# Performance work log

Hardware: AMD Instinct MI355X
Metric: run time of the kernel (lower is better)

## Reference

```python
import jax, jax.numpy as jnp
import numpy as np

B, N = 256, 2000          # clouds, points per cloud
M1, M2 = 100, 5           # fps sample counts (ratio 0.05 twice)
K1, K2 = 20, 20           # neighbors per cluster (= 1/ratio)
R1, R2, R3 = 0.3, 1.0, 2.0
F1, F2, F3 = 5, 25, 45


def _fps(pts, m):
    # iterative farthest point sampling, deterministic start at index 0
    n = pts.shape[0]
    def step(carry, _):
        mind, last = carry
        d = jnp.sum((pts - pts[last]) ** 2, axis=-1)
        mind = jnp.minimum(mind, d)
        return (mind, jnp.argmax(mind).astype(jnp.int32)), last
    _, idx = jax.lax.scan(step, (jnp.full((n,), 1e10, pts.dtype), jnp.int32(0)), None, length=m)
    return idx


def _radius_knn(q, pts, k, r):
    # k nearest neighbors of each query, masked to the radius ball (static-shape gnn.radius)
    d = jnp.sum((q[:, None, :] - pts[None, :, :]) ** 2, axis=-1)  # (M, n)
    negd, idx = jax.lax.top_k(-d, k)
    return idx, (-negd) <= r * r


def _masked_max(h, mask):
    return jnp.max(jnp.where(mask[..., None], h, -1e10), axis=1)


def _forward(points, W1, b1, W2, b2, W3, b3, D1, bD1, D2, bD2, D3, bD3):
    def per_cloud(pts):
        # ---- encode level 1 ----
        samples = pts[_fps(pts, M1)]                              # (M1,3)
        idx1, m1 = _radius_knn(samples, pts, K1, R1)
        rel = (pts[idx1] - samples[:, None, :]) / R1 * m1[..., None]   # (M1,K1,3)
        f1 = _masked_max(jax.nn.relu(rel @ W1 + b1), m1)          # (M1,F1)
        # ---- encode level 2 ----
        samples2 = samples[_fps(samples, M2)]                     # (M2,3)
        idx2, m2 = _radius_knn(samples2, samples, K2, R2)
        rel2 = (samples[idx2] - samples2[:, None, :]) / R2 * m2[..., None]
        h2 = jax.nn.relu(jnp.concatenate([rel2, f1[idx2]], axis=-1) @ W2 + b2)
        f2 = _masked_max(h2, m2)                                  # (M2,F2)
        # ---- encode level 3 (global) ----
        rel3 = samples2 / R3
        h3 = jax.nn.relu(jnp.concatenate([rel3, f2], axis=-1) @ W3 + b3)
        latent = jnp.max(h3, axis=0)                              # (F3,)
        # ---- hierarchical decode ----
        o1 = (latent @ D1 + bD1).reshape(M2, 3 + F2)
        dec, cf = o1[:, :3], jax.nn.relu(o1[:, 3:])               # (M2,3),(M2,F2)
        o2 = (cf @ D2 + bD2).reshape(M2 * K2, 3 + F1)
        dec2, cf2 = o2[:, :3], jax.nn.relu(o2[:, 3:])             # (M2*K2,3/F1)
        dec3 = (cf2 @ D3 + bD3).reshape(M2 * K2 * K1, 3)
        # ---- reconstruction: repeat_interleave + add + scale ----
        s2_out = dec * R3
        s_out = (jnp.repeat(s2_out, K2, axis=0) + dec2) * R2
        return (jnp.repeat(s_out, K1, axis=0) + dec3) * R1        # (N,3)
    return jax.vmap(per_cloud)(points).reshape(B * N, 3)


def setup_inputs():
    key = jax.random.key(0)
    ks = jax.random.split(key, 8)
    p = lambda k, s: jax.random.normal(k, s, jnp.float32) * 0.1
    z = lambda s: jnp.zeros((s,), jnp.float32)
    return {
        "points": jax.random.normal(ks[0], (B, N, 3), jnp.float32),
        "W1": p(ks[1], (3, F1)), "b1": z(F1),
        "W2": p(ks[2], (3 + F1, F2)), "b2": z(F2),
        "W3": p(ks[3], (3 + F2, F3)), "b3": z(F3),
        "D1": p(ks[4], (F3, M2 * (3 + F2))), "bD1": z(M2 * (3 + F2)),
        "D2": p(ks[5], (F2, K2 * (3 + F1))), "bD2": z(K2 * (3 + F1)),
        "D3": p(ks[6], (F1, K1 * 3)), "bD3": z(K1 * 3),
    }


def reference(points, W1, b1, W2, b2, W3, b3, D1, bD1, D2, bD2, D3, bD3):
    return _forward(points, W1, b1, W2, b2, W3, b3, D1, bD1, D2, bD2, D3, bD3)
```

## Files before the change

kernel.cpp:

```cpp
#include <hip/hip_runtime.h>

#define TPB 512
#define NW 8
#define NPTS 2000
#define M1C 100
#define M2C 5
#define KNN 20
#define CAP 64
#define CANDCAP 128

__device__ __forceinline__ float dist3(float px, float py, float pz,
                                       float qx, float qy, float qz) {
#pragma clang fp contract(off)
    float dx = px - qx, dy = py - qy, dz = pz - qz;
    return dx * dx + dy * dy + dz * dz;
}
__device__ __forceinline__ float dist3d(float px, float py, float pz,
                                        float qx, float qy, float qz,
                                        float& dx, float& dy, float& dz) {
#pragma clang fp contract(off)
    dx = px - qx; dy = py - qy; dz = pz - qz;
    return dx * dx + dy * dy + dz * dz;
}

#define ARGMAX_STEP(ctrl, rm)                                                        \
    do {                                                                             \
        float ov = __int_as_float(__builtin_amdgcn_update_dpp(                       \
            (int)0xff800000, __float_as_int(v), ctrl, rm, 0xf, false));              \
        int oi = __builtin_amdgcn_update_dpp(0x7fffffff, i, ctrl, rm, 0xf, false);   \
        bool take = (ov > v) || (ov == v && oi < i);                                 \
        v = take ? ov : v;                                                           \
        i = take ? oi : i;                                                           \
    } while (0)

__device__ __forceinline__ void wave_argmax(float& v, int& i) {
    ARGMAX_STEP(0x111, 0xf);
    ARGMAX_STEP(0x112, 0xf);
    ARGMAX_STEP(0x114, 0xf);
    ARGMAX_STEP(0x118, 0xf);
    ARGMAX_STEP(0x142, 0xa);
    ARGMAX_STEP(0x143, 0xc);
    v = __int_as_float(__builtin_amdgcn_readlane(__float_as_int(v), 63));
    i = __builtin_amdgcn_readlane(i, 63);
}

#define FMAX_STEP(ctrl, rm)                                                          \
    do {                                                                             \
        float _t = __int_as_float(__builtin_amdgcn_update_dpp(                       \
            (int)0xff800000, __float_as_int(x), ctrl, rm, 0xf, false));              \
        x = fmaxf(x, _t);                                                            \
    } while (0)

__device__ __forceinline__ float wave_fmax(float x) {
    FMAX_STEP(0x111, 0xf);
    FMAX_STEP(0x112, 0xf);
    FMAX_STEP(0x114, 0xf);
    FMAX_STEP(0x118, 0xf);
    FMAX_STEP(0x142, 0xa);
    FMAX_STEP(0x143, 0xc);
    return __int_as_float(__builtin_amdgcn_readlane(__float_as_int(x), 63));
}

__global__ __launch_bounds__(TPB) void pointnet_kernel(
    const float* __restrict__ P,
    const float* __restrict__ W1, const float* __restrict__ b1,
    const float* __restrict__ W2, const float* __restrict__ b2,
    const float* __restrict__ W3, const float* __restrict__ b3,
    const float* __restrict__ D1, const float* __restrict__ bD1,
    const float* __restrict__ D2, const float* __restrict__ bD2,
    const float* __restrict__ D3, const float* __restrict__ bD3,
    float* __restrict__ out)
{
    __shared__ float sP[3][NPTS];
    __shared__ float smpx[M1C], smpy[M1C], smpz[M1C];
    __shared__ float s2x[M2C], s2y[M2C], s2z[M2C];
    __shared__ int   cnt[M1C];
    __shared__ float candd[M1C * CAP];
    __shared__ int   candi[M1C * CAP];
    __shared__ float f1s[M1C][5];
    __shared__ float f2s[M2C][25];
    __shared__ float latent[45];
    __shared__ float decv[M2C][3];
    __shared__ float cfs[M2C][25];
    __shared__ float dec2s[M1C][3];
    __shared__ float cf2s[M1C][5];
    __shared__ float kn2d[NW][CANDCAP];
    __shared__ int   kn2i[NW][CANDCAP];
    __shared__ __align__(16) float rvv[2][NW];
    __shared__ __align__(16) int   rvi[2][NW];
    __shared__ float w2s[200], b2s[25], w3s[1260], b3s[45];

    const int b = blockIdx.x;
    const int tid = threadIdx.x;
    const int lane = tid & 63;
    const int wid = tid >> 6;
    float* sx = sP[0]; float* sy = sP[1]; float* sz = sP[2];

    const float R1SQ = (float)(0.3 * 0.3);
    const float R2SQ = 1.0f;
    const float INVR1 = 1.0f / 0.3f;

    const float* Pb = P + (size_t)b * (NPTS * 3);
    const float4* P4 = (const float4*)Pb;
    for (int i = tid; i < (NPTS * 3) / 4; i += TPB) {
        float4 f = P4[i];
        int j = 4 * i;
        float v[4] = {f.x, f.y, f.z, f.w};
#pragma unroll
        for (int e = 0; e < 4; ++e) {
            int jj = j + e;
            (&sP[0][0])[(jj % 3) * NPTS + jj / 3] = v[e];
        }
    }
    for (int t = tid; t < M1C; t += TPB) cnt[t] = 0;
    for (int t = tid; t < 200; t += TPB) w2s[t] = W2[t];
    for (int t = tid; t < 25; t += TPB) b2s[t] = b2[t];
    for (int t = tid; t < 1260; t += TPB) w3s[t] = W3[t];
    for (int t = tid; t < 45; t += TPB) b3s[t] = b3[t];
    float rw1[15], rb1[5];
#pragma unroll
    for (int i = 0; i < 15; ++i) rw1[i] = W1[i];
#pragma unroll
    for (int i = 0; i < 5; ++i) rb1[i] = b1[i];
    __syncthreads();

    float px[4], py[4], pz[4], mind[4];
#pragma unroll
    for (int k = 0; k < 4; ++k) {
        int j = tid + (k << 9);
        bool v = j < NPTS;
        int jc = v ? j : 0;
        px[k] = v ? sx[jc] : 1e18f;
        py[k] = v ? sy[jc] : 1e18f;
        pz[k] = v ? sz[jc] : 1e18f;
        mind[k] = v ? 1e10f : -1.0f;
    }

    float qx = sx[0], qy = sy[0], qz = sz[0];
    for (int it = 0; it < M1C; ++it) {
        if (tid == 0) { smpx[it] = qx; smpy[it] = qy; smpz[it] = qz; }
        float bv = -1.0f; int bi = 0x7fffffff;
#pragma unroll
        for (int k = 0; k < 4; ++k) {
            int j = tid + (k << 9);
            float dx, dy, dz;
            float d = dist3d(px[k], py[k], pz[k], qx, qy, qz, dx, dy, dz);
            float m = fminf(mind[k], d);
            mind[k] = m;
            if (m > bv) { bv = m; bi = j; }
            if (d <= R1SQ) {
                int pos = atomicAdd(&cnt[it], 1);
                if (pos < CAP) { candd[it * CAP + pos] = d; candi[it * CAP + pos] = j; }
            }
        }
        if (it == M1C - 1) break;
        wave_argmax(bv, bi);
        int p = it & 1;
        if (lane == 0) { rvv[p][wid] = bv; rvi[p][wid] = bi; }
        __syncthreads();
        float4 va = *(const float4*)&rvv[p][0];
        float4 vb = *(const float4*)&rvv[p][4];
        int4 ia = *(const int4*)&rvi[p][0];
        int4 ib = *(const int4*)&rvi[p][4];
        float cv = va.x; int ci = ia.x;
#define SEL(vv, ii) { bool t = ((vv) > cv) || ((vv) == cv && (ii) < ci); cv = t ? (vv) : cv; ci = t ? (ii) : ci; }
        SEL(va.y, ia.y) SEL(va.z, ia.z) SEL(va.w, ia.w)
        SEL(vb.x, ib.x) SEL(vb.y, ib.y) SEL(vb.z, ib.z) SEL(vb.w, ib.w)
#undef SEL
        qx = sx[ci]; qy = sy[ci]; qz = sz[ci];
    }
    __syncthreads();

    if (wid == 0) {
        float ax = smpx[lane], ay = smpy[lane], az = smpz[lane];
        bool vb2 = lane < (M1C - 64);
        float bx2 = vb2 ? smpx[lane + 64] : 1e18f;
        float by2 = vb2 ? smpy[lane + 64] : 1e18f;
        float bz2 = vb2 ? smpz[lane + 64] : 1e18f;
        float m2a = 1e10f;
        float m2b = vb2 ? 1e10f : -1.0f;
        int last2 = 0;
        for (int it = 0; it < M2C; ++it) {
            float fx = smpx[last2], fy = smpy[last2], fz = smpz[last2];
            if (lane == 0) { s2x[it] = fx; s2y[it] = fy; s2z[it] = fz; }
            m2a = fminf(m2a, dist3(ax, ay, az, fx, fy, fz));
            m2b = fminf(m2b, dist3(bx2, by2, bz2, fx, fy, fz));
            float v = m2a; int i = lane;
            if (m2b > v) { v = m2b; i = lane + 64; }
            wave_argmax(v, i);
            last2 = i;
        }
    } else {
        for (int s = wid - 1; s < M1C; s += (NW - 1)) {
            int cn = cnt[s];
            float qx2 = smpx[s], qy2 = smpy[s], qz2 = smpz[s];
            float fmx[5];
#pragma unroll
            for (int f = 0; f < 5; ++f) fmx[f] = -1e30f;
            if (cn <= CAP) {
                if (lane < cn) {
                    float d = candd[s * CAP + lane];
                    int j = candi[s * CAP + lane];
                    bool valid = true;
                    if (cn > KNN) {
                        int rank = 0;
                        for (int u = 0; u < cn; ++u) {
                            float du = candd[s * CAP + u];
                            int iu = candi[s * CAP + u];
                            rank += (du < d || (du == d && iu < j)) ? 1 : 0;
                        }
                        valid = rank < KNN;
                    }
                    if (valid) {
                        float rx = (sx[j] - qx2) * INVR1;
                        float ry = (sy[j] - qy2) * INVR1;
                        float rz = (sz[j] - qz2) * INVR1;
#pragma unroll
                        for (int f = 0; f < 5; ++f) {
                            float h = fmaf(rx, rw1[f], fmaf(ry, rw1[5 + f], fmaf(rz, rw1[10 + f], rb1[f])));
                            fmx[f] = fmaxf(fmx[f], fmaxf(h, 0.0f));
                        }
                    }
                }
            } else {
                int cn2 = 0;
                for (int c = 0; c < 32; ++c) {
                    int j = c * 64 + lane;
                    float d = 0.0f; bool pred = false;
                    if (j < NPTS) {
                        d = dist3(sx[j], sy[j], sz[j], qx2, qy2, qz2);
                        pred = (d <= R1SQ);
                    }
                    unsigned long long mb = __ballot(pred);
                    if (pred) {
                        int pos = cn2 + (int)__popcll(mb & ((1ull << lane) - 1ull));
                        if (pos < CANDCAP) { kn2d[wid][pos] = d; kn2i[wid][pos] = j; }
                    }
                    cn2 += (int)__popcll(mb);
                }
                if (cn2 > CANDCAP) cn2 = CANDCAP;
                for (int t = lane; t < cn2; t += 64) {
                    float d = kn2d[wid][t]; int j = kn2i[wid][t];
                    int rank = 0;
                    for (int u = 0; u < cn2; ++u) {
                        float du = kn2d[wid][u]; int iu = kn2i[wid][u];
                        rank += (du < d || (du == d && iu < j)) ? 1 : 0;
                    }
                    if (rank < KNN) {
                        float rx = (sx[j] - qx2) * INVR1;
                        float ry = (sy[j] - qy2) * INVR1;
                        float rz = (sz[j] - qz2) * INVR1;
#pragma unroll
                        for (int f = 0; f < 5; ++f) {
                            float h = fmaf(rx, rw1[f], fmaf(ry, rw1[5 + f], fmaf(rz, rw1[10 + f], rb1[f])));
                            fmx[f] = fmaxf(fmx[f], fmaxf(h, 0.0f));
                        }
                    }
                }
            }
#pragma unroll
            for (int f = 0; f < 5; ++f) {
                float mx = wave_fmax(fmx[f]);
                if (lane == 0) f1s[s][f] = mx;
            }
        }
    }
    __syncthreads();

    for (int s = wid; s < M2C; s += NW) {
        float qx2 = s2x[s], qy2 = s2y[s], qz2 = s2z[s];
        int cn = 0;
#pragma unroll
        for (int c = 0; c < 2; ++c) {
            int j = c * 64 + lane;
            float d = 0.0f; bool pred = false;
            if (j < M1C) {
                d = dist3(smpx[j], smpy[j], smpz[j], qx2, qy2, qz2);
                pred = (d <= R2SQ);
            }
            unsigned long long mb = __ballot(pred);
            if (pred) {
                int pos = cn + (int)__popcll(mb & ((1ull << lane) - 1ull));
                kn2d[wid][pos] = d; kn2i[wid][pos] = j;
            }
            cn += (int)__popcll(mb);
        }
        float hmx[25];
#pragma unroll
        for (int f = 0; f < 25; ++f) hmx[f] = -1e30f;
        for (int t = lane; t < cn; t += 64) {
            float d = kn2d[wid][t]; int j = kn2i[wid][t];
            bool valid = true;
            if (cn > KNN) {
                int rank = 0;
                for (int u = 0; u < cn; ++u) {
                    float du = kn2d[wid][u]; int iu = kn2i[wid][u];
                    rank += (du < d || (du == d && iu < j)) ? 1 : 0;
                }
                valid = rank < KNN;
            }
            if (valid) {
                float in8[8];
                in8[0] = smpx[j] - qx2; in8[1] = smpy[j] - qy2; in8[2] = smpz[j] - qz2;
#pragma unroll
                for (int f = 0; f < 5; ++f) in8[3 + f] = f1s[j][f];
#pragma unroll
                for (int f = 0; f < 25; ++f) {
                    float h = b2s[f];
#pragma unroll
                    for (int i = 0; i < 8; ++i) h = fmaf(in8[i], w2s[i * 25 + f], h);
                    hmx[f] = fmaxf(hmx[f], fmaxf(h, 0.0f));
                }
            }
        }
#pragma unroll
        for (int f = 0; f < 25; ++f) {
            float mx = wave_fmax(hmx[f]);
            if (lane == 0) f2s[s][f] = mx;
        }
    }
    __syncthreads();

    if (wid == 0 && lane < 45) {
        float lm = -1e30f;
        for (int r = 0; r < M2C; ++r) {
            float h = b3s[lane];
            h = fmaf(s2x[r] * 0.5f, w3s[0 * 45 + lane], h);
            h = fmaf(s2y[r] * 0.5f, w3s[1 * 45 + lane], h);
            h = fmaf(s2z[r] * 0.5f, w3s[2 * 45 + lane], h);
#pragma unroll
            for (int i = 0; i < 25; ++i) h = fmaf(f2s[r][i], w3s[(3 + i) * 45 + lane], h);
            lm = fmaxf(lm, fmaxf(h, 0.0f));
        }
        latent[lane] = lm;
    }
    __syncthreads();

    for (int t = tid; t < 140; t += TPB) {
        float acc = bD1[t];
        for (int i = 0; i < 45; i++) acc = fmaf(latent[i], D1[i * 140 + t], acc);
        int r = t / 28, c = t % 28;
        if (c < 3) decv[r][c] = acc;
        else cfs[r][c - 3] = fmaxf(acc, 0.0f);
    }
    __syncthreads();

    for (int t = tid; t < 800; t += TPB) {
        int r = t / 160, c = t % 160;
        float acc = bD2[c];
        for (int i = 0; i < 25; i++) acc = fmaf(cfs[r][i], D2[i * 160 + c], acc);
        int g = r * 20 + c / 8, c8 = c % 8;
        if (c8 < 3) dec2s[g][c8] = acc;
        else cf2s[g][c8 - 3] = fmaxf(acc, 0.0f);
    }
    __syncthreads();

    float* outb = out + (size_t)b * (NPTS * 3);
    for (int t = tid; t < NPTS * 3; t += TPB) {
        int n = t / 3, c = t % 3;
        int g = n / 20;
        int m = n / 400;
        int r60 = (n % 20) * 3 + c;
        float acc = bD3[r60];
        for (int i = 0; i < 5; i++) acc = fmaf(cf2s[g][i], D3[i * 60 + r60], acc);
        float val = ((decv[m][c] * 2.0f + dec2s[g][c]) + acc) * 0.3f;
        outb[t] = val;
    }
}

extern "C" void kernel_launch(void* const* d_in, const int* in_sizes, int n_in,
                              void* d_out, int out_size, void* d_ws, size_t ws_size,
                              hipStream_t stream) {
    const float* P   = (const float*)d_in[0];
    const float* W1  = (const float*)d_in[1];
    const float* b1  = (const float*)d_in[2];
    const float* W2  = (const float*)d_in[3];
    const float* b2  = (const float*)d_in[4];
    const float* W3  = (const float*)d_in[5];
    const float* b3  = (const float*)d_in[6];
    const float* D1  = (const float*)d_in[7];
    const float* bD1 = (const float*)d_in[8];
    const float* D2  = (const float*)d_in[9];
    const float* bD2 = (const float*)d_in[10];
    const float* D3  = (const float*)d_in[11];
    const float* bD3 = (const float*)d_in[12];
    float* out = (float*)d_out;

    int B = in_sizes[0] / (NPTS * 3);
    hipLaunchKernelGGL(pointnet_kernel, dim3(B), dim3(TPB), 0, stream,
                       P, W1, b1, W2, b2, W3, b3, D1, bD1, D2, bD2, D3, bD3, out);
}
```

Baseline: 219.8 us.

## Split fused kernel into FPS, grouping, and decode kernels via workspace

```diff
diff --git a/kernel.cpp b/kernel.cpp
--- a/kernel.cpp
+++ b/kernel.cpp
@@ -8,6 +8,15 @@
 #define KNN 20
 #define CAP 64
 #define CANDCAP 128
+
+#define CSTR 4120
+#define OF_SMPX 0
+#define OF_SMPY 100
+#define OF_SMPZ 200
+#define OF_S2   300
+#define OF_F1   320
+#define OF_CNT  820
+#define OF_CANDI 920
 
 __device__ __forceinline__ float dist3(float px, float py, float pz,
                                        float qx, float qy, float qz) {
@@ -61,44 +70,22 @@
     return __int_as_float(__builtin_amdgcn_readlane(__float_as_int(x), 63));
 }
 
-__global__ __launch_bounds__(TPB) void pointnet_kernel(
-    const float* __restrict__ P,
-    const float* __restrict__ W1, const float* __restrict__ b1,
-    const float* __restrict__ W2, const float* __restrict__ b2,
-    const float* __restrict__ W3, const float* __restrict__ b3,
-    const float* __restrict__ D1, const float* __restrict__ bD1,
-    const float* __restrict__ D2, const float* __restrict__ bD2,
-    const float* __restrict__ D3, const float* __restrict__ bD3,
-    float* __restrict__ out)
+__global__ __launch_bounds__(TPB) void kernelA(const float* __restrict__ P,
+                                               float* __restrict__ ws)
 {
     __shared__ float sP[3][NPTS];
+    __shared__ unsigned short candi16[M1C * CAP];
+    __shared__ int cnt[M1C];
     __shared__ float smpx[M1C], smpy[M1C], smpz[M1C];
-    __shared__ float s2x[M2C], s2y[M2C], s2z[M2C];
-    __shared__ int   cnt[M1C];
-    __shared__ float candd[M1C * CAP];
-    __shared__ int   candi[M1C * CAP];
-    __shared__ float f1s[M1C][5];
-    __shared__ float f2s[M2C][25];
-    __shared__ float latent[45];
-    __shared__ float decv[M2C][3];
-    __shared__ float cfs[M2C][25];
-    __shared__ float dec2s[M1C][3];
-    __shared__ float cf2s[M1C][5];
-    __shared__ float kn2d[NW][CANDCAP];
-    __shared__ int   kn2i[NW][CANDCAP];
-    __shared__ __align__(16) float rvv[2][NW];
-    __shared__ __align__(16) int   rvi[2][NW];
-    __shared__ float w2s[200], b2s[25], w3s[1260], b3s[45];
+    __shared__ __align__(16) float4 sA[2][NW];
+    __shared__ __align__(16) float sZ[2][NW];
 
     const int b = blockIdx.x;
     const int tid = threadIdx.x;
     const int lane = tid & 63;
     const int wid = tid >> 6;
     float* sx = sP[0]; float* sy = sP[1]; float* sz = sP[2];
-
     const float R1SQ = (float)(0.3 * 0.3);
-    const float R2SQ = 1.0f;
-    const float INVR1 = 1.0f / 0.3f;
 
     const float* Pb = P + (size_t)b * (NPTS * 3);
     const float4* P4 = (const float4*)Pb;
@@ -113,15 +100,6 @@
         }
     }
     for (int t = tid; t < M1C; t += TPB) cnt[t] = 0;
-    for (int t = tid; t < 200; t += TPB) w2s[t] = W2[t];
-    for (int t = tid; t < 25; t += TPB) b2s[t] = b2[t];
-    for (int t = tid; t < 1260; t += TPB) w3s[t] = W3[t];
-    for (int t = tid; t < 45; t += TPB) b3s[t] = b3[t];
-    float rw1[15], rb1[5];
-#pragma unroll
-    for (int i = 0; i < 15; ++i) rw1[i] = W1[i];
-#pragma unroll
-    for (int i = 0; i < 5; ++i) rb1[i] = b1[i];
     __syncthreads();
 
     float px[4], py[4], pz[4], mind[4];
@@ -150,27 +128,41 @@
             if (m > bv) { bv = m; bi = j; }
             if (d <= R1SQ) {
                 int pos = atomicAdd(&cnt[it], 1);
-                if (pos < CAP) { candd[it * CAP + pos] = d; candi[it * CAP + pos] = j; }
+                if (pos < CAP) candi16[it * CAP + pos] = (unsigned short)j;
             }
         }
         if (it == M1C - 1) break;
+        float lv = bv; int li = bi;
         wave_argmax(bv, bi);
         int p = it & 1;
-        if (lane == 0) { rvv[p][wid] = bv; rvi[p][wid] = bi; }
+        if (lv == bv && li == bi) {
+            int k = bi >> 9;
+            float cx = k == 0 ? px[0] : k == 1 ? px[1] : k == 2 ? px[2] : px[3];
+            float cy = k == 0 ? py[0] : k == 1 ? py[1] : k == 2 ? py[2] : py[3];
+            float cz = k == 0 ? pz[0] : k == 1 ? pz[1] : k == 2 ? pz[2] : pz[3];
+            sA[p][wid] = make_float4(bv, __int_as_float(bi), cx, cy);
+            sZ[p][wid] = cz;
+        }
         __syncthreads();
-        float4 va = *(const float4*)&rvv[p][0];
-        float4 vb = *(const float4*)&rvv[p][4];
-        int4 ia = *(const int4*)&rvi[p][0];
-        int4 ib = *(const int4*)&rvi[p][4];
-        float cv = va.x; int ci = ia.x;
-#define SEL(vv, ii) { bool t = ((vv) > cv) || ((vv) == cv && (ii) < ci); cv = t ? (vv) : cv; ci = t ? (ii) : ci; }
-        SEL(va.y, ia.y) SEL(va.z, ia.z) SEL(va.w, ia.w)
-        SEL(vb.x, ib.x) SEL(vb.y, ib.y) SEL(vb.z, ib.z) SEL(vb.w, ib.w)
+        float4 a0 = sA[p][0], a1 = sA[p][1], a2 = sA[p][2], a3 = sA[p][3];
+        float4 a4 = sA[p][4], a5 = sA[p][5], a6 = sA[p][6], a7 = sA[p][7];
+        float4 z0 = *(const float4*)&sZ[p][0];
+        float4 z1 = *(const float4*)&sZ[p][4];
+        float cv = a0.x; int ci = __float_as_int(a0.y);
+        qx = a0.z; qy = a0.w; qz = z0.x;
+#define SEL(aw, zz)                                                                  \
+        {                                                                            \
+            int ii = __float_as_int(aw.y);                                           \
+            bool t = (aw.x > cv) || (aw.x == cv && ii < ci);                         \
+            if (t) { cv = aw.x; ci = ii; qx = aw.z; qy = aw.w; qz = zz; }            \
+        }
+        SEL(a1, z0.y) SEL(a2, z0.z) SEL(a3, z0.w)
+        SEL(a4, z1.x) SEL(a5, z1.y) SEL(a6, z1.z) SEL(a7, z1.w)
 #undef SEL
-        qx = sx[ci]; qy = sy[ci]; qz = sz[ci];
-    }
-    __syncthreads();
-
+    }
+    __syncthreads();
+
+    size_t cs = (size_t)b * CSTR;
     if (wid == 0) {
         float ax = smpx[lane], ay = smpy[lane], az = smpz[lane];
         bool vb2 = lane < (M1C - 64);
@@ -182,7 +174,11 @@
         int last2 = 0;
         for (int it = 0; it < M2C; ++it) {
             float fx = smpx[last2], fy = smpy[last2], fz = smpz[last2];
-            if (lane == 0) { s2x[it] = fx; s2y[it] = fy; s2z[it] = fz; }
+            if (lane == 0) {
+                ws[cs + OF_S2 + it] = fx;
+                ws[cs + OF_S2 + 5 + it] = fy;
+                ws[cs + OF_S2 + 10 + it] = fz;
+            }
             m2a = fminf(m2a, dist3(ax, ay, az, fx, fy, fz));
             m2b = fminf(m2b, dist3(bx2, by2, bz2, fx, fy, fz));
             float v = m2a; int i = lane;
@@ -191,80 +187,169 @@
             last2 = i;
         }
     } else {
-        for (int s = wid - 1; s < M1C; s += (NW - 1)) {
-            int cn = cnt[s];
-            float qx2 = smpx[s], qy2 = smpy[s], qz2 = smpz[s];
-            float fmx[5];
-#pragma unroll
-            for (int f = 0; f < 5; ++f) fmx[f] = -1e30f;
-            if (cn <= CAP) {
-                if (lane < cn) {
-                    float d = candd[s * CAP + lane];
-                    int j = candi[s * CAP + lane];
-                    bool valid = true;
-                    if (cn > KNN) {
-                        int rank = 0;
-                        for (int u = 0; u < cn; ++u) {
-                            float du = candd[s * CAP + u];
-                            int iu = candi[s * CAP + u];
-                            rank += (du < d || (du == d && iu < j)) ? 1 : 0;
-                        }
-                        valid = rank < KNN;
-                    }
-                    if (valid) {
-                        float rx = (sx[j] - qx2) * INVR1;
-                        float ry = (sy[j] - qy2) * INVR1;
-                        float rz = (sz[j] - qz2) * INVR1;
-#pragma unroll
-                        for (int f = 0; f < 5; ++f) {
-                            float h = fmaf(rx, rw1[f], fmaf(ry, rw1[5 + f], fmaf(rz, rw1[10 + f], rb1[f])));
-                            fmx[f] = fmaxf(fmx[f], fmaxf(h, 0.0f));
-                        }
-                    }
+        int t2 = tid - 64;
+        for (int t = t2; t < M1C; t += TPB - 64) {
+            ws[cs + OF_SMPX + t] = smpx[t];
+            ws[cs + OF_SMPY + t] = smpy[t];
+            ws[cs + OF_SMPZ + t] = smpz[t];
+            ((int*)ws)[cs + OF_CNT + t] = cnt[t];
+        }
+        const unsigned* ca = (const unsigned*)candi16;
+        unsigned* wsu = (unsigned*)ws;
+        for (int t = t2; t < M1C * CAP / 2; t += TPB - 64)
+            wsu[cs + OF_CANDI + t] = ca[t];
+    }
+}
+
+__global__ __launch_bounds__(TPB) void kernelB(const float* __restrict__ P,
+                                               const float* __restrict__ W1,
+                                               const float* __restrict__ b1,
+                                               float* __restrict__ ws, int nPairs)
+{
+    __shared__ float cdw[NW][CANDCAP];
+    __shared__ int ciw[NW][CANDCAP];
+    const int tid = threadIdx.x;
+    const int lane = tid & 63;
+    const int wid = tid >> 6;
+    int id = blockIdx.x * NW + wid;
+    if (id >= nPairs) return;
+    int cloud = id / M1C;
+    int s = id - cloud * M1C;
+    size_t cs = (size_t)cloud * CSTR;
+    const float* Pc = P + (size_t)cloud * (NPTS * 3);
+    const float R1SQ = (float)(0.3 * 0.3);
+    const float INVR1 = 1.0f / 0.3f;
+
+    float qx = ws[cs + OF_SMPX + s];
+    float qy = ws[cs + OF_SMPY + s];
+    float qz = ws[cs + OF_SMPZ + s];
+    int cn = ((const int*)ws)[cs + OF_CNT + s];
+    float rw1[15], rb1[5];
+#pragma unroll
+    for (int i = 0; i < 15; ++i) rw1[i] = W1[i];
+#pragma unroll
+    for (int i = 0; i < 5; ++i) rb1[i] = b1[i];
+    float fmx[5];
+#pragma unroll
+    for (int f = 0; f < 5; ++f) fmx[f] = -1e30f;
+
+    if (cn <= CAP) {
+        const unsigned short* ci16 = (const unsigned short*)(ws + cs + OF_CANDI);
+        int j = 0; float d = 0.0f;
+        bool act = lane < cn;
+        if (act) {
+            j = ci16[s * CAP + lane];
+            d = dist3(Pc[3 * j], Pc[3 * j + 1], Pc[3 * j + 2], qx, qy, qz);
+            cdw[wid][lane] = d; ciw[wid][lane] = j;
+        }
+        if (act) {
+            bool valid = true;
+            if (cn > KNN) {
+                int rank = 0;
+                for (int u = 0; u < cn; ++u) {
+                    float du = cdw[wid][u]; int iu = ciw[wid][u];
+                    rank += (du < d || (du == d && iu < j)) ? 1 : 0;
                 }
-            } else {
-                int cn2 = 0;
-                for (int c = 0; c < 32; ++c) {
-                    int j = c * 64 + lane;
-                    float d = 0.0f; bool pred = false;
-                    if (j < NPTS) {
-                        d = dist3(sx[j], sy[j], sz[j], qx2, qy2, qz2);
-                        pred = (d <= R1SQ);
-                    }
-                    unsigned long long mb = __ballot(pred);
-                    if (pred) {
-                        int pos = cn2 + (int)__popcll(mb & ((1ull << lane) - 1ull));
-                        if (pos < CANDCAP) { kn2d[wid][pos] = d; kn2i[wid][pos] = j; }
-                    }
-                    cn2 += (int)__popcll(mb);
+                valid = rank < KNN;
+            }
+            if (valid) {
+                float rx = (Pc[3 * j] - qx) * INVR1;
+                float ry = (Pc[3 * j + 1] - qy) * INVR1;
+                float rz = (Pc[3 * j + 2] - qz) * INVR1;
+#pragma unroll
+                for (int f = 0; f < 5; ++f) {
+                    float h = fmaf(rx, rw1[f], fmaf(ry, rw1[5 + f], fmaf(rz, rw1[10 + f], rb1[f])));
+                    fmx[f] = fmaxf(fmx[f], fmaxf(h, 0.0f));
                 }
-                if (cn2 > CANDCAP) cn2 = CANDCAP;
-                for (int t = lane; t < cn2; t += 64) {
-                    float d = kn2d[wid][t]; int j = kn2i[wid][t];
-                    int rank = 0;
-                    for (int u = 0; u < cn2; ++u) {
-                        float du = kn2d[wid][u]; int iu = kn2i[wid][u];
-                        rank += (du < d || (du == d && iu < j)) ? 1 : 0;
-                    }
-                    if (rank < KNN) {
-                        float rx = (sx[j] - qx2) * INVR1;
-                        float ry = (sy[j] - qy2) * INVR1;
-                        float rz = (sz[j] - qz2) * INVR1;
-#pragma unroll
-                        for (int f = 0; f < 5; ++f) {
-                            float h = fmaf(rx, rw1[f], fmaf(ry, rw1[5 + f], fmaf(rz, rw1[10 + f], rb1[f])));
-                            fmx[f] = fmaxf(fmx[f], fmaxf(h, 0.0f));
-                        }
-                    }
+            }
+        }
+    } else {
+        int cn2 = 0;
+        for (int c = 0; c < 32; ++c) {
+            int j2 = c * 64 + lane;
+            float d2 = 0.0f; bool pred = false;
+            if (j2 < NPTS) {
+                d2 = dist3(Pc[3 * j2], Pc[3 * j2 + 1], Pc[3 * j2 + 2], qx, qy, qz);
+                pred = (d2 <= R1SQ);
+            }
+            unsigned long long mb = __ballot(pred);
+            if (pred) {
+                int pos = cn2 + (int)__popcll(mb & ((1ull << lane) - 1ull));
+                if (pos < CANDCAP) { cdw[wid][pos] = d2; ciw[wid][pos] = j2; }
+            }
+            cn2 += (int)__popcll(mb);
+        }
+        if (cn2 > CANDCAP) cn2 = CANDCAP;
+        for (int t = lane; t < cn2; t += 64) {
+            float d = cdw[wid][t]; int j = ciw[wid][t];
+            int rank = 0;
+            for (int u = 0; u < cn2; ++u) {
+                float du = cdw[wid][u]; int iu = ciw[wid][u];
+                rank += (du < d || (du == d && iu < j)) ? 1 : 0;
+            }
+            if (rank < KNN) {
+                float rx = (Pc[3 * j] - qx) * INVR1;
+                float ry = (Pc[3 * j + 1] - qy) * INVR1;
+                float rz = (Pc[3 * j + 2] - qz) * INVR1;
+#pragma unroll
+                for (int f = 0; f < 5; ++f) {
+                    float h = fmaf(rx, rw1[f], fmaf(ry, rw1[5 + f], fmaf(rz, rw1[10 + f], rb1[f])));
+                    fmx[f] = fmaxf(fmx[f], fmaxf(h, 0.0f));
                 }
             }
-#pragma unroll
-            for (int f = 0; f < 5; ++f) {
-                float mx = wave_fmax(fmx[f]);
-                if (lane == 0) f1s[s][f] = mx;
-            }
-        }
-    }
+        }
+    }
+#pragma unroll
+    for (int f = 0; f < 5; ++f) fmx[f] = wave_fmax(fmx[f]);
+    if (lane == 0) {
+#pragma unroll
+        for (int f = 0; f < 5; ++f) ws[cs + OF_F1 + s * 5 + f] = fmx[f];
+    }
+}
+
+__global__ __launch_bounds__(TPB) void kernelC(
+    const float* __restrict__ W2, const float* __restrict__ b2,
+    const float* __restrict__ W3, const float* __restrict__ b3,
+    const float* __restrict__ D1, const float* __restrict__ bD1,
+    const float* __restrict__ D2, const float* __restrict__ bD2,
+    const float* __restrict__ D3, const float* __restrict__ bD3,
+    const float* __restrict__ ws, float* __restrict__ out)
+{
+    __shared__ float smpx[M1C], smpy[M1C], smpz[M1C];
+    __shared__ float s2x[M2C], s2y[M2C], s2z[M2C];
+    __shared__ float f1s[M1C][5];
+    __shared__ float f2s[M2C][25];
+    __shared__ float latent[45];
+    __shared__ float decv[M2C][3];
+    __shared__ float cfs[M2C][25];
+    __shared__ float dec2s[M1C][3];
+    __shared__ float cf2s[M1C][5];
+    __shared__ float kn2d[NW][CANDCAP];
+    __shared__ int   kn2i[NW][CANDCAP];
+    __shared__ float w2s[200], b2s[25], w3s[1260], b3s[45];
+
+    const int b = blockIdx.x;
+    const int tid = threadIdx.x;
+    const int lane = tid & 63;
+    const int wid = tid >> 6;
+    size_t cs = (size_t)b * CSTR;
+    const float R2SQ = 1.0f;
+
+    for (int t = tid; t < M1C; t += TPB) {
+        smpx[t] = ws[cs + OF_SMPX + t];
+        smpy[t] = ws[cs + OF_SMPY + t];
+        smpz[t] = ws[cs + OF_SMPZ + t];
+    }
+    for (int t = tid; t < M2C; t += TPB) {
+        s2x[t] = ws[cs + OF_S2 + t];
+        s2y[t] = ws[cs + OF_S2 + 5 + t];
+        s2z[t] = ws[cs + OF_S2 + 10 + t];
+    }
+    for (int t = tid; t < M1C * 5; t += TPB) ((float*)f1s)[t] = ws[cs + OF_F1 + t];
+    for (int t = tid; t < 200; t += TPB) w2s[t] = W2[t];
+    for (int t = tid; t < 25; t += TPB) b2s[t] = b2[t];
+    for (int t = tid; t < 1260; t += TPB) w3s[t] = W3[t];
+    for (int t = tid; t < 45; t += TPB) b3s[t] = b3[t];
     __syncthreads();
 
     for (int s = wid; s < M2C; s += NW) {
@@ -385,8 +470,13 @@
     const float* D3  = (const float*)d_in[11];
     const float* bD3 = (const float*)d_in[12];
     float* out = (float*)d_out;
+    float* ws = (float*)d_ws;
 
     int B = in_sizes[0] / (NPTS * 3);
-    hipLaunchKernelGGL(pointnet_kernel, dim3(B), dim3(TPB), 0, stream,
-                       P, W1, b1, W2, b2, W3, b3, D1, bD1, D2, bD2, D3, bD3, out);
-}
+    int nPairs = B * M1C;
+    hipLaunchKernelGGL(kernelA, dim3(B), dim3(TPB), 0, stream, P, ws);
+    hipLaunchKernelGGL(kernelB, dim3((nPairs + NW - 1) / NW), dim3(TPB), 0, stream,
+                       P, W1, b1, ws, nPairs);
+    hipLaunchKernelGGL(kernelC, dim3(B), dim3(TPB), 0, stream,
+                       W2, b2, W3, b3, D1, bD1, D2, bD2, D3, bD3, ws, out);
+}
```

After: 247.1 us. +12.4%, slower.

## Split FPS into separate lean kernel and recompute radius neighbors in second kernel

Applied to the files above, without the earlier changes.

```diff
diff --git a/kernel.cpp b/kernel.cpp
--- a/kernel.cpp
+++ b/kernel.cpp
@@ -2,24 +2,24 @@
 
 #define TPB 512
 #define NW 8
+#define TPBA 256
+#define NWA 4
 #define NPTS 2000
 #define M1C 100
 #define M2C 5
 #define KNN 20
-#define CAP 64
 #define CANDCAP 128
+
+#define CSTR 320
+#define OF_SMPX 0
+#define OF_SMPY 100
+#define OF_SMPZ 200
+#define OF_S2   300
 
 __device__ __forceinline__ float dist3(float px, float py, float pz,
                                        float qx, float qy, float qz) {
 #pragma clang fp contract(off)
     float dx = px - qx, dy = py - qy, dz = pz - qz;
-    return dx * dx + dy * dy + dz * dz;
-}
-__device__ __forceinline__ float dist3d(float px, float py, float pz,
-                                        float qx, float qy, float qz,
-                                        float& dx, float& dy, float& dz) {
-#pragma clang fp contract(off)
-    dx = px - qx; dy = py - qy; dz = pz - qz;
     return dx * dx + dy * dy + dz * dz;
 }
 
@@ -61,34 +61,13 @@
     return __int_as_float(__builtin_amdgcn_readlane(__float_as_int(x), 63));
 }
 
-__global__ __launch_bounds__(TPB) void pointnet_kernel(
-    const float* __restrict__ P,
-    const float* __restrict__ W1, const float* __restrict__ b1,
-    const float* __restrict__ W2, const float* __restrict__ b2,
-    const float* __restrict__ W3, const float* __restrict__ b3,
-    const float* __restrict__ D1, const float* __restrict__ bD1,
-    const float* __restrict__ D2, const float* __restrict__ bD2,
-    const float* __restrict__ D3, const float* __restrict__ bD3,
-    float* __restrict__ out)
+__global__ __launch_bounds__(TPBA) void kernelA(const float* __restrict__ P,
+                                                float* __restrict__ ws)
 {
     __shared__ float sP[3][NPTS];
     __shared__ float smpx[M1C], smpy[M1C], smpz[M1C];
-    __shared__ float s2x[M2C], s2y[M2C], s2z[M2C];
-    __shared__ int   cnt[M1C];
-    __shared__ float candd[M1C * CAP];
-    __shared__ int   candi[M1C * CAP];
-    __shared__ float f1s[M1C][5];
-    __shared__ float f2s[M2C][25];
-    __shared__ float latent[45];
-    __shared__ float decv[M2C][3];
-    __shared__ float cfs[M2C][25];
-    __shared__ float dec2s[M1C][3];
-    __shared__ float cf2s[M1C][5];
-    __shared__ float kn2d[NW][CANDCAP];
-    __shared__ int   kn2i[NW][CANDCAP];
-    __shared__ __align__(16) float rvv[2][NW];
-    __shared__ __align__(16) int   rvi[2][NW];
-    __shared__ float w2s[200], b2s[25], w3s[1260], b3s[45];
+    __shared__ __align__(16) float4 sA[2][NWA];
+    __shared__ __align__(16) float sZ[2][NWA];
 
     const int b = blockIdx.x;
     const int tid = threadIdx.x;
@@ -96,13 +75,9 @@
     const int wid = tid >> 6;
     float* sx = sP[0]; float* sy = sP[1]; float* sz = sP[2];
 
-    const float R1SQ = (float)(0.3 * 0.3);
-    const float R2SQ = 1.0f;
-    const float INVR1 = 1.0f / 0.3f;
-
     const float* Pb = P + (size_t)b * (NPTS * 3);
     const float4* P4 = (const float4*)Pb;
-    for (int i = tid; i < (NPTS * 3) / 4; i += TPB) {
+    for (int i = tid; i < (NPTS * 3) / 4; i += TPBA) {
         float4 f = P4[i];
         int j = 4 * i;
         float v[4] = {f.x, f.y, f.z, f.w};
@@ -112,22 +87,12 @@
             (&sP[0][0])[(jj % 3) * NPTS + jj / 3] = v[e];
         }
     }
-    for (int t = tid; t < M1C; t += TPB) cnt[t] = 0;
-    for (int t = tid; t < 200; t += TPB) w2s[t] = W2[t];
-    for (int t = tid; t < 25; t += TPB) b2s[t] = b2[t];
-    for (int t = tid; t < 1260; t += TPB) w3s[t] = W3[t];
-    for (int t = tid; t < 45; t += TPB) b3s[t] = b3[t];
-    float rw1[15], rb1[5];
-#pragma unroll
-    for (int i = 0; i < 15; ++i) rw1[i] = W1[i];
-#pragma unroll
-    for (int i = 0; i < 5; ++i) rb1[i] = b1[i];
-    __syncthreads();
-
-    float px[4], py[4], pz[4], mind[4];
-#pragma unroll
-    for (int k = 0; k < 4; ++k) {
-        int j = tid + (k << 9);
+    __syncthreads();
+
+    float px[8], py[8], pz[8], mind[8];
+#pragma unroll
+    for (int k = 0; k < 8; ++k) {
+        int j = tid + (k << 8);
         bool v = j < NPTS;
         int jc = v ? j : 0;
         px[k] = v ? sx[jc] : 1e18f;
@@ -141,36 +106,46 @@
         if (tid == 0) { smpx[it] = qx; smpy[it] = qy; smpz[it] = qz; }
         float bv = -1.0f; int bi = 0x7fffffff;
 #pragma unroll
-        for (int k = 0; k < 4; ++k) {
-            int j = tid + (k << 9);
-            float dx, dy, dz;
-            float d = dist3d(px[k], py[k], pz[k], qx, qy, qz, dx, dy, dz);
+        for (int k = 0; k < 8; ++k) {
+            float d = dist3(px[k], py[k], pz[k], qx, qy, qz);
             float m = fminf(mind[k], d);
             mind[k] = m;
-            if (m > bv) { bv = m; bi = j; }
-            if (d <= R1SQ) {
-                int pos = atomicAdd(&cnt[it], 1);
-                if (pos < CAP) { candd[it * CAP + pos] = d; candi[it * CAP + pos] = j; }
-            }
+            if (m > bv) { bv = m; bi = tid + (k << 8); }
         }
         if (it == M1C - 1) break;
+        float lv = bv; int li = bi;
         wave_argmax(bv, bi);
         int p = it & 1;
-        if (lane == 0) { rvv[p][wid] = bv; rvi[p][wid] = bi; }
+        if (lv == bv && li == bi) {
+            int k = bi >> 8;
+            float cx = px[0], cy = py[0], cz = pz[0];
+#pragma unroll
+            for (int kk = 1; kk < 8; ++kk) {
+                bool t = (k == kk);
+                cx = t ? px[kk] : cx;
+                cy = t ? py[kk] : cy;
+                cz = t ? pz[kk] : cz;
+            }
+            sA[p][wid] = make_float4(bv, __int_as_float(bi), cx, cy);
+            sZ[p][wid] = cz;
+        }
         __syncthreads();
-        float4 va = *(const float4*)&rvv[p][0];
-        float4 vb = *(const float4*)&rvv[p][4];
-        int4 ia = *(const int4*)&rvi[p][0];
-        int4 ib = *(const int4*)&rvi[p][4];
-        float cv = va.x; int ci = ia.x;
-#define SEL(vv, ii) { bool t = ((vv) > cv) || ((vv) == cv && (ii) < ci); cv = t ? (vv) : cv; ci = t ? (ii) : ci; }
-        SEL(va.y, ia.y) SEL(va.z, ia.z) SEL(va.w, ia.w)
-        SEL(vb.x, ib.x) SEL(vb.y, ib.y) SEL(vb.z, ib.z) SEL(vb.w, ib.w)
+        float4 a0 = sA[p][0], a1 = sA[p][1], a2 = sA[p][2], a3 = sA[p][3];
+        float4 z0 = *(const float4*)&sZ[p][0];
+        float cv = a0.x; int ci = __float_as_int(a0.y);
+        qx = a0.z; qy = a0.w; qz = z0.x;
+#define SEL(aw, zz)                                                                  \
+        {                                                                            \
+            int ii = __float_as_int(aw.y);                                           \
+            bool t = (aw.x > cv) || (aw.x == cv && ii < ci);                         \
+            if (t) { cv = aw.x; ci = ii; qx = aw.z; qy = aw.w; qz = zz; }            \
+        }
+        SEL(a1, z0.y) SEL(a2, z0.z) SEL(a3, z0.w)
 #undef SEL
-        qx = sx[ci]; qy = sy[ci]; qz = sz[ci];
-    }
-    __syncthreads();
-
+    }
+    __syncthreads();
+
+    size_t cs = (size_t)b * CSTR;
     if (wid == 0) {
         float ax = smpx[lane], ay = smpy[lane], az = smpz[lane];
         bool vb2 = lane < (M1C - 64);
@@ -182,7 +157,11 @@
         int last2 = 0;
         for (int it = 0; it < M2C; ++it) {
             float fx = smpx[last2], fy = smpy[last2], fz = smpz[last2];
-            if (lane == 0) { s2x[it] = fx; s2y[it] = fy; s2z[it] = fz; }
+            if (lane == 0) {
+                ws[cs + OF_S2 + it] = fx;
+                ws[cs + OF_S2 + 5 + it] = fy;
+                ws[cs + OF_S2 + 10 + it] = fz;
+            }
             m2a = fminf(m2a, dist3(ax, ay, az, fx, fy, fz));
             m2b = fminf(m2b, dist3(bx2, by2, bz2, fx, fy, fz));
             float v = m2a; int i = lane;
@@ -191,78 +170,131 @@
             last2 = i;
         }
     } else {
-        for (int s = wid - 1; s < M1C; s += (NW - 1)) {
-            int cn = cnt[s];
-            float qx2 = smpx[s], qy2 = smpy[s], qz2 = smpz[s];
-            float fmx[5];
-#pragma unroll
-            for (int f = 0; f < 5; ++f) fmx[f] = -1e30f;
-            if (cn <= CAP) {
-                if (lane < cn) {
-                    float d = candd[s * CAP + lane];
-                    int j = candi[s * CAP + lane];
-                    bool valid = true;
-                    if (cn > KNN) {
-                        int rank = 0;
-                        for (int u = 0; u < cn; ++u) {
-                            float du = candd[s * CAP + u];
-                            int iu = candi[s * CAP + u];
-                            rank += (du < d || (du == d && iu < j)) ? 1 : 0;
-                        }
-                        valid = rank < KNN;
-                    }
-                    if (valid) {
-                        float rx = (sx[j] - qx2) * INVR1;
-                        float ry = (sy[j] - qy2) * INVR1;
-                        float rz = (sz[j] - qz2) * INVR1;
-#pragma unroll
-                        for (int f = 0; f < 5; ++f) {
-                            float h = fmaf(rx, rw1[f], fmaf(ry, rw1[5 + f], fmaf(rz, rw1[10 + f], rb1[f])));
-                            fmx[f] = fmaxf(fmx[f], fmaxf(h, 0.0f));
-                        }
-                    }
+        int t2 = tid - 64;
+        for (int t = t2; t < M1C; t += TPBA - 64) {
+            ws[cs + OF_SMPX + t] = smpx[t];
+            ws[cs + OF_SMPY + t] = smpy[t];
+            ws[cs + OF_SMPZ + t] = smpz[t];
+        }
+    }
+}
+
+__global__ __launch_bounds__(TPB) void kernelBC(
+    const float* __restrict__ P,
+    const float* __restrict__ W1, const float* __restrict__ b1,
+    const float* __restrict__ W2, const float* __restrict__ b2,
+    const float* __restrict__ W3, const float* __restrict__ b3,
+    const float* __restrict__ D1, const float* __restrict__ bD1,
+    const float* __restrict__ D2, const float* __restrict__ bD2,
+    const float* __restrict__ D3, const float* __restrict__ bD3,
+    const float* __restrict__ ws, float* __restrict__ out)
+{
+    __shared__ float sP[3][NPTS];
+    __shared__ float smpx[M1C], smpy[M1C], smpz[M1C];
+    __shared__ float s2x[M2C], s2y[M2C], s2z[M2C];
+    __shared__ float f1s[M1C][5];
+    __shared__ float f2s[M2C][25];
+    __shared__ float latent[45];
+    __shared__ float decv[M2C][3];
+    __shared__ float cfs[M2C][25];
+    __shared__ float dec2s[M1C][3];
+    __shared__ float cf2s[M1C][5];
+    __shared__ float knd[NW][CANDCAP];
+    __shared__ int   kni[NW][CANDCAP];
+    __shared__ float w2s[200], b2s[25], w3s[1260], b3s[45];
+
+    const int b = blockIdx.x;
+    const int tid = threadIdx.x;
+    const int lane = tid & 63;
+    const int wid = tid >> 6;
+    float* sx = sP[0]; float* sy = sP[1]; float* sz = sP[2];
+    size_t cs = (size_t)b * CSTR;
+
+    const float R1SQ = (float)(0.3 * 0.3);
+    const float R2SQ = 1.0f;
+    const float INVR1 = 1.0f / 0.3f;
+
+    const float* Pb = P + (size_t)b * (NPTS * 3);
+    const float4* P4 = (const float4*)Pb;
+    for (int i = tid; i < (NPTS * 3) / 4; i += TPB) {
+        float4 f = P4[i];
+        int j = 4 * i;
+        float v[4] = {f.x, f.y, f.z, f.w};
+#pragma unroll
+        for (int e = 0; e < 4; ++e) {
+            int jj = j + e;
+            (&sP[0][0])[(jj % 3) * NPTS + jj / 3] = v[e];
+        }
+    }
+    for (int t = tid; t < M1C; t += TPB) {
+        smpx[t] = ws[cs + OF_SMPX + t];
+        smpy[t] = ws[cs + OF_SMPY + t];
+        smpz[t] = ws[cs + OF_SMPZ + t];
+    }
+    for (int t = tid; t < M2C; t += TPB) {
+        s2x[t] = ws[cs + OF_S2 + t];
+        s2y[t] = ws[cs + OF_S2 + 5 + t];
+        s2z[t] = ws[cs + OF_S2 + 10 + t];
+    }
+    for (int t = tid; t < 200; t += TPB) w2s[t] = W2[t];
+    for (int t = tid; t < 25; t += TPB) b2s[t] = b2[t];
+    for (int t = tid; t < 1260; t += TPB) w3s[t] = W3[t];
+    for (int t = tid; t < 45; t += TPB) b3s[t] = b3[t];
+    float rw1[15], rb1[5];
+#pragma unroll
+    for (int i = 0; i < 15; ++i) rw1[i] = W1[i];
+#pragma unroll
+    for (int i = 0; i < 5; ++i) rb1[i] = b1[i];
+    __syncthreads();
+
+    for (int s = wid; s < M1C; s += NW) {
+        float qx = smpx[s], qy = smpy[s], qz = smpz[s];
+        int cn = 0;
+#pragma unroll 4
+        for (int c = 0; c < 32; ++c) {
+            int j = c * 64 + lane;
+            float d = 0.0f; bool pred = false;
+            if (j < NPTS) {
+                d = dist3(sx[j], sy[j], sz[j], qx, qy, qz);
+                pred = (d <= R1SQ);
+            }
+            unsigned long long mb = __ballot(pred);
+            if (pred) {
+                int pos = cn + (int)__popcll(mb & ((1ull << lane) - 1ull));
+                if (pos < CANDCAP) { knd[wid][pos] = d; kni[wid][pos] = j; }
+            }
+            cn += (int)__popcll(mb);
+        }
+        if (cn > CANDCAP) cn = CANDCAP;
+        float fmx[5];
+#pragma unroll
+        for (int f = 0; f < 5; ++f) fmx[f] = -1e30f;
+        for (int t = lane; t < cn; t += 64) {
+            float d = knd[wid][t]; int j = kni[wid][t];
+            bool valid = true;
+            if (cn > KNN) {
+                int rank = 0;
+                for (int u = 0; u < cn; ++u) {
+                    float du = knd[wid][u]; int iu = kni[wid][u];
+                    rank += (du < d || (du == d && iu < j)) ? 1 : 0;
                 }
-            } else {
-                int cn2 = 0;
-                for (int c = 0; c < 32; ++c) {
-                    int j = c * 64 + lane;
-                    float d = 0.0f; bool pred = false;
-                    if (j < NPTS) {
-                        d = dist3(sx[j], sy[j], sz[j], qx2, qy2, qz2);
-                        pred = (d <= R1SQ);
-                    }
-                    unsigned long long mb = __ballot(pred);
-                    if (pred) {
-                        int pos = cn2 + (int)__popcll(mb & ((1ull << lane) - 1ull));
-                        if (pos < CANDCAP) { kn2d[wid][pos] = d; kn2i[wid][pos] = j; }
-                    }
-                    cn2 += (int)__popcll(mb);
+                valid = rank < KNN;
+            }
+            if (valid) {
+                float rx = (sx[j] - qx) * INVR1;
+                float ry = (sy[j] - qy) * INVR1;
+                float rz = (sz[j] - qz) * INVR1;
+#pragma unroll
+                for (int f = 0; f < 5; ++f) {
+                    float h = fmaf(rx, rw1[f], fmaf(ry, rw1[5 + f], fmaf(rz, rw1[10 + f], rb1[f])));
+                    fmx[f] = fmaxf(fmx[f], fmaxf(h, 0.0f));
                 }
-                if (cn2 > CANDCAP) cn2 = CANDCAP;
-                for (int t = lane; t < cn2; t += 64) {
-                    float d = kn2d[wid][t]; int j = kn2i[wid][t];
-                    int rank = 0;
-                    for (int u = 0; u < cn2; ++u) {
-                        float du = kn2d[wid][u]; int iu = kn2i[wid][u];
-                        rank += (du < d || (du == d && iu < j)) ? 1 : 0;
-                    }
-                    if (rank < KNN) {
-                        float rx = (sx[j] - qx2) * INVR1;
-                        float ry = (sy[j] - qy2) * INVR1;
-                        float rz = (sz[j] - qz2) * INVR1;
-#pragma unroll
-                        for (int f = 0; f < 5; ++f) {
-                            float h = fmaf(rx, rw1[f], fmaf(ry, rw1[5 + f], fmaf(rz, rw1[10 + f], rb1[f])));
-                            fmx[f] = fmaxf(fmx[f], fmaxf(h, 0.0f));
-                        }
-                    }
-                }
-            }
-#pragma unroll
-            for (int f = 0; f < 5; ++f) {
-                float mx = wave_fmax(fmx[f]);
-                if (lane == 0) f1s[s][f] = mx;
-            }
+            }
+        }
+#pragma unroll
+        for (int f = 0; f < 5; ++f) {
+            float mx = wave_fmax(fmx[f]);
+            if (lane == 0) f1s[s][f] = mx;
         }
     }
     __syncthreads();
@@ -281,7 +313,7 @@
             unsigned long long mb = __ballot(pred);
             if (pred) {
                 int pos = cn + (int)__popcll(mb & ((1ull << lane) - 1ull));
-                kn2d[wid][pos] = d; kn2i[wid][pos] = j;
+                knd[wid][pos] = d; kni[wid][pos] = j;
             }
             cn += (int)__popcll(mb);
         }
@@ -289,12 +321,12 @@
 #pragma unroll
         for (int f = 0; f < 25; ++f) hmx[f] = -1e30f;
         for (int t = lane; t < cn; t += 64) {
-            float d = kn2d[wid][t]; int j = kn2i[wid][t];
+            float d = knd[wid][t]; int j = kni[wid][t];
             bool valid = true;
             if (cn > KNN) {
                 int rank = 0;
                 for (int u = 0; u < cn; ++u) {
-                    float du = kn2d[wid][u]; int iu = kn2i[wid][u];
+                    float du = knd[wid][u]; int iu = kni[wid][u];
                     rank += (du < d || (du == d && iu < j)) ? 1 : 0;
                 }
                 valid = rank < KNN;
@@ -385,8 +417,10 @@
     const float* D3  = (const float*)d_in[11];
     const float* bD3 = (const float*)d_in[12];
     float* out = (float*)d_out;
+    float* ws = (float*)d_ws;
 
     int B = in_sizes[0] / (NPTS * 3);
-    hipLaunchKernelGGL(pointnet_kernel, dim3(B), dim3(TPB), 0, stream,
-                       P, W1, b1, W2, b2, W3, b3, D1, bD1, D2, bD2, D3, bD3, out);
-}
+    hipLaunchKernelGGL(kernelA, dim3(B), dim3(TPBA), 0, stream, P, ws);
+    hipLaunchKernelGGL(kernelBC, dim3(B), dim3(TPB), 0, stream,
+                       P, W1, b1, W2, b2, W3, b3, D1, bD1, D2, bD2, D3, bD3, ws, out);
+}
```

Result: slower. 237.3 us (+7.9%).
